# Kernel optimization log

Measured on AMD Instinct MI355X. Metric: run time of the kernel, lower is better.

## Reference

```python
import jax, jax.numpy as jnp
import numpy as np

B, C, H, W = 8, 256, 64, 64
CQK = C // 8


def setup_inputs() -> dict:
    key = jax.random.key(0)
    ks = jax.random.split(key, 9)
    s_in = 1.0 / np.sqrt(C)
    return {
        "feature1": jax.random.normal(ks[0], (B, C, H, W), jnp.float32),
        "feature2": jax.random.normal(ks[1], (B, C, H, W), jnp.float32),
        "feature3": jax.random.normal(ks[2], (B, C, H, W), jnp.float32),
        # 1x1 conv weights stored as [out_ch, in_ch]
        "wq": jax.random.uniform(ks[3], (CQK, C), jnp.float32, -s_in, s_in),
        "bq": jax.random.uniform(ks[4], (CQK,), jnp.float32, -s_in, s_in),
        "wk": jax.random.uniform(ks[5], (CQK, C), jnp.float32, -s_in, s_in),
        "bk": jax.random.uniform(ks[6], (CQK,), jnp.float32, -s_in, s_in),
        "wv": jax.random.uniform(ks[7], (C, C), jnp.float32, -s_in, s_in),
        "bv": jax.random.uniform(ks[8], (C,), jnp.float32, -s_in, s_in),
    }


def reference(feature1, feature2, feature3, wq, bq, wk, bk, wv, bv):
    b, c, h, w = feature1.shape
    hw = h * w
    # 1x1 convs == per-pixel channel GEMMs
    q = jnp.einsum('bchw,oc->bohw', feature1, wq) + bq[None, :, None, None]
    k = jnp.einsum('bchw,oc->bohw', feature2, wk) + bk[None, :, None, None]
    v = jnp.einsum('bchw,oc->bohw', feature3, wv) + bv[None, :, None, None]
    q = q.reshape(b, -1, hw).transpose(0, 2, 1)  # [b, hw, cqk]
    k = k.reshape(b, -1, hw)                      # [b, cqk, hw]
    v = v.reshape(b, -1, hw)                      # [b, c, hw]
    attn = jax.nn.softmax(jnp.einsum('bnc,bcm->bnm', q, k), axis=-1)  # [b, hw, hw]
    # fused = value @ attn^T  -> [b, c, hw]
    fused = jnp.einsum('bcm,bnm->bcn', v, attn)
    return fused.reshape(b, c, h, w)
```

## Files before the change

### kernel.cpp

```cpp
#include <hip/hip_runtime.h>
#include <math.h>

#define BATCH 8
#define CH    256
#define HWPIX 4096
#define CQK_  32

typedef __bf16 bf16x8 __attribute__((ext_vector_type(8)));
typedef __bf16 bf16x4 __attribute__((ext_vector_type(4)));
typedef __bf16 bf16x2 __attribute__((ext_vector_type(2)));
typedef float  f32x4  __attribute__((ext_vector_type(4)));

#define FS_STR 68

static __device__ inline bf16x8 ld_frag(const __bf16* p) {
  bf16x4 lo = *(const bf16x4*)p;
  bf16x4 hi = *(const bf16x4*)(p + 4);
  return __builtin_shufflevector(lo, hi, 0, 1, 2, 3, 4, 5, 6, 7);
}

static __device__ inline bf16x8 w_frag(const float* p) {
  const float4 a = *(const float4*)p;
  const float4 b = *(const float4*)(p + 4);
  bf16x8 r;
  r[0] = (__bf16)a.x; r[1] = (__bf16)a.y; r[2] = (__bf16)a.z; r[3] = (__bf16)a.w;
  r[4] = (__bf16)b.x; r[5] = (__bf16)b.y; r[6] = (__bf16)b.z; r[7] = (__bf16)b.w;
  return r;
}

__global__ __launch_bounds__(256, 4) void proj_all(
    const float* __restrict__ f1, const float* __restrict__ f2,
    const float* __restrict__ f3,
    const float* __restrict__ wq, const float* __restrict__ bq,
    const float* __restrict__ wk, const float* __restrict__ bk,
    const float* __restrict__ wv, const float* __restrict__ bv,
    __bf16* __restrict__ qT, __bf16* __restrict__ kT, __bf16* __restrict__ vv)
{
  __shared__ __align__(16) __bf16 f_s[2][64 * FS_STR];
  const int t    = threadIdx.x;
  const int w    = __builtin_amdgcn_readfirstlane(t >> 6);
  const int lane = t & 63;
  const int q16  = lane & 15;
  const int quad = lane >> 4;
  const int b    = blockIdx.z;
  const int n0   = blockIdx.x * 64;
  const int mode = blockIdx.y;

  const int sn  = (t & 15) * 4;
  const int scp = (t >> 4) * 2;
#define STAGE(fb, c0, dst)                                                      \
  {                                                                             \
    _Pragma("unroll") for (int rr = 0; rr < 2; ++rr) {                          \
      const int c = rr * 32 + scp;                                              \
      const float4 a0 = *(const float4*)&(fb)[(size_t)((c0) + c) * HWPIX + sn]; \
      const float4 a1 = *(const float4*)&(fb)[(size_t)((c0) + c + 1) * HWPIX + sn]; \
      _Pragma("unroll") for (int i = 0; i < 4; ++i) {                           \
        bf16x2 pk;                                                              \
        pk[0] = (__bf16)((const float*)&a0)[i];                                 \
        pk[1] = (__bf16)((const float*)&a1)[i];                                 \
        *(bf16x2*)&(dst)[(sn + i) * FS_STR + c] = pk;                           \
      }                                                                         \
    }                                                                           \
  }

  if (mode == 0) {
    const float* f1b = f1 + (size_t)b * CH * HWPIX + n0;
    const float* f2b = f2 + (size_t)b * CH * HWPIX + n0;
    f32x4 accQ[2], accK[2];
#pragma unroll
    for (int i = 0; i < 2; ++i) {
      accQ[i] = (f32x4){0.f, 0.f, 0.f, 0.f};
      accK[i] = (f32x4){0.f, 0.f, 0.f, 0.f};
    }
    for (int c0 = 0; c0 < CH; c0 += 64) {
      STAGE(f1b, c0, f_s[0]);
      STAGE(f2b, c0, f_s[1]);
      __syncthreads();
      bf16x8 afQ[2], afK[2];
#pragma unroll
      for (int kh = 0; kh < 2; ++kh) {
        afQ[kh] = ld_frag(&f_s[0][(16 * w + q16) * FS_STR + 32 * kh + quad * 8]);
        afK[kh] = ld_frag(&f_s[1][(16 * w + q16) * FS_STR + 32 * kh + quad * 8]);
      }
#pragma unroll
      for (int ot = 0; ot < 2; ++ot) {
#pragma unroll
        for (int kh = 0; kh < 2; ++kh) {
          const bf16x8 wfq =
              w_frag(wq + (size_t)(16 * ot + q16) * CH + c0 + 32 * kh + quad * 8);
          accQ[ot] = __builtin_amdgcn_mfma_f32_16x16x32_bf16(afQ[kh], wfq, accQ[ot], 0, 0, 0);
          const bf16x8 wfk =
              w_frag(wk + (size_t)(16 * ot + q16) * CH + c0 + 32 * kh + quad * 8);
          accK[ot] = __builtin_amdgcn_mfma_f32_16x16x32_bf16(afK[kh], wfk, accK[ot], 0, 0, 0);
        }
      }
      __syncthreads();
    }
    const float bq0 = bq[q16], bq1 = bq[16 + q16];
    const float bk0 = bk[q16], bk1 = bk[16 + q16];
#pragma unroll
    for (int r = 0; r < 4; ++r) {
      const size_t row = (size_t)b * HWPIX + n0 + 16 * w + quad * 4 + r;
      qT[row * CQK_ + q16]      = (__bf16)(accQ[0][r] + bq0);
      qT[row * CQK_ + 16 + q16] = (__bf16)(accQ[1][r] + bq1);
      kT[row * CQK_ + q16]      = (__bf16)(accK[0][r] + bk0);
      kT[row * CQK_ + 16 + q16] = (__bf16)(accK[1][r] + bk1);
    }
  } else {
    const int cbase = (mode - 1) * 128;
    const float* f3b = f3 + (size_t)b * CH * HWPIX + n0;
    f32x4 acc[2][4];
#pragma unroll
    for (int ct = 0; ct < 2; ++ct)
#pragma unroll
      for (int nt = 0; nt < 4; ++nt) acc[ct][nt] = (f32x4){0.f, 0.f, 0.f, 0.f};

    for (int c0 = 0; c0 < CH; c0 += 64) {
      STAGE(f3b, c0, f_s[0]);
      __syncthreads();
      bf16x8 af[2][2];
#pragma unroll
      for (int ct = 0; ct < 2; ++ct)
#pragma unroll
        for (int kh = 0; kh < 2; ++kh)
          af[ct][kh] = w_frag(wv + (size_t)(cbase + 64 * ct + 16 * w + q16) * CH
                              + c0 + 32 * kh + quad * 8);
#pragma unroll
      for (int nt = 0; nt < 4; ++nt) {
#pragma unroll
        for (int kh = 0; kh < 2; ++kh) {
          const bf16x8 bfr = ld_frag(&f_s[0][(16 * nt + q16) * FS_STR + 32 * kh + quad * 8]);
#pragma unroll
          for (int ct = 0; ct < 2; ++ct)
            acc[ct][nt] = __builtin_amdgcn_mfma_f32_16x16x32_bf16(
                af[ct][kh], bfr, acc[ct][nt], 0, 0, 0);
        }
      }
      __syncthreads();
    }
#pragma unroll
    for (int ct = 0; ct < 2; ++ct) {
      const float4 bi = *(const float4*)&bv[cbase + 64 * ct + 16 * w + quad * 4];
#pragma unroll
      for (int nt = 0; nt < 4; ++nt) {
#pragma unroll
        for (int r = 0; r < 4; ++r) {
          const int c = cbase + 64 * ct + 16 * w + quad * 4 + r;
          vv[((size_t)b * CH + c) * HWPIX + n0 + 16 * nt + q16] =
              (__bf16)(acc[ct][nt][r] + ((const float*)&bi)[r]);
        }
      }
    }
  }
#undef STAGE
}

__global__ __launch_bounds__(256, 2) void attn_kernel(
    const __bf16* __restrict__ qT, const __bf16* __restrict__ kT,
    const __bf16* __restrict__ vv, float* __restrict__ out)
{
  __shared__ __align__(16) __bf16 p_s[2][64 * 72];
  __shared__ float L_s[64];

  const int t    = threadIdx.x;
  const int w    = __builtin_amdgcn_readfirstlane(t >> 6);
  const int lane = t & 63;
  const int q16  = lane & 15;
  const int quad = lane >> 4;

  const int b  = blockIdx.x & 7;
  const int q0 = (blockIdx.x >> 3) * 64;

  const __bf16* kTb = kT + (size_t)b * HWPIX * CQK_;
  const int koff = q16 * CQK_ + quad * 8;

  const __bf16* vp[4];
#pragma unroll
  for (int ct = 0; ct < 4; ++ct)
    vp[ct] = vv + ((size_t)b * CH + 64 * w + 16 * ct + q16) * HWPIX + quad * 8;

  const bf16x8 qfrag =
      *(const bf16x8*)(qT + ((size_t)b * HWPIX + q0 + 16 * w + q16) * CQK_ + quad * 8);

  f32x4 oacc[4][4];
#pragma unroll
  for (int i = 0; i < 4; ++i)
#pragma unroll
    for (int j = 0; j < 4; ++j)
      oacc[i][j] = (f32x4){0.f, 0.f, 0.f, 0.f};
  float Lp[4] = {0.f, 0.f, 0.f, 0.f};

  bf16x8 kf[4];
#pragma unroll
  for (int mt = 0; mt < 4; ++mt)
    kf[mt] = *(const bf16x8*)(kTb + koff + mt * 512);
  {
    f32x4 Sv[4];
#pragma unroll
    for (int mt = 0; mt < 4; ++mt)
      Sv[mt] = __builtin_amdgcn_mfma_f32_16x16x32_bf16(
          qfrag, kf[mt], (f32x4){0.f, 0.f, 0.f, 0.f}, 0, 0, 0);
    const __bf16* kb1 = kTb + 64 * CQK_;
#pragma unroll
    for (int mt = 0; mt < 4; ++mt)
      kf[mt] = *(const bf16x8*)(kb1 + koff + mt * 512);
#pragma unroll
    for (int mt = 0; mt < 4; ++mt) {
#pragma unroll
      for (int r = 0; r < 4; ++r) {
        const float e = __expf(Sv[mt][r]);
        Lp[r] += e;
        p_s[0][(16 * w + quad * 4 + r) * 72 + 16 * mt + q16] = (__bf16)e;
      }
    }
  }
  __syncthreads();

  for (int i = 0; i < 64; ++i) {
    bf16x8 vf[4][2];
#pragma unroll
    for (int ct = 0; ct < 4; ++ct)
#pragma unroll
      for (int mh = 0; mh < 2; ++mh)
        vf[ct][mh] = *(const bf16x8*)(vp[ct] + mh * 32);

    const __bf16* pb = p_s[i & 1];
    bf16x8 pf[4][2];
#pragma unroll
    for (int nt = 0; nt < 4; ++nt)
#pragma unroll
      for (int mh = 0; mh < 2; ++mh)
        pf[nt][mh] = *(const bf16x8*)(&pb[(16 * nt + q16) * 72 + 32 * mh + quad * 8]);

    if (i < 63) {
      f32x4 Sv[4];
#pragma unroll
      for (int mt = 0; mt < 4; ++mt)
        Sv[mt] = __builtin_amdgcn_mfma_f32_16x16x32_bf16(
            qfrag, kf[mt], (f32x4){0.f, 0.f, 0.f, 0.f}, 0, 0, 0);
      const __bf16* kb2 = kTb + (size_t)((i + 2) & 63) * (64 * CQK_);
#pragma unroll
      for (int mt = 0; mt < 4; ++mt)
        kf[mt] = *(const bf16x8*)(kb2 + koff + mt * 512);
      __bf16* pw = p_s[(i + 1) & 1];
#pragma unroll
      for (int mt = 0; mt < 4; ++mt) {
#pragma unroll
        for (int r = 0; r < 4; ++r) {
          const float e = __expf(Sv[mt][r]);
          Lp[r] += e;
          pw[(16 * w + quad * 4 + r) * 72 + 16 * mt + q16] = (__bf16)e;
        }
      }
    }

#pragma unroll
    for (int ct = 0; ct < 4; ++ct)
#pragma unroll
      for (int nt = 0; nt < 4; ++nt)
#pragma unroll
        for (int mh = 0; mh < 2; ++mh)
          oacc[ct][nt] = __builtin_amdgcn_mfma_f32_16x16x32_bf16(
              vf[ct][mh], pf[nt][mh], oacc[ct][nt], 0, 0, 0);

#pragma unroll
    for (int ct = 0; ct < 4; ++ct) vp[ct] += 64;
    __syncthreads();
  }

#pragma unroll
  for (int r = 0; r < 4; ++r) {
    Lp[r] += __shfl_xor(Lp[r], 1);
    Lp[r] += __shfl_xor(Lp[r], 2);
    Lp[r] += __shfl_xor(Lp[r], 4);
    Lp[r] += __shfl_xor(Lp[r], 8);
  }
  if (q16 == 0) {
#pragma unroll
    for (int r = 0; r < 4; ++r) L_s[16 * w + quad * 4 + r] = Lp[r];
  }
  __syncthreads();

  float rinv[4];
#pragma unroll
  for (int nt = 0; nt < 4; ++nt) rinv[nt] = 1.0f / L_s[16 * nt + q16];

  float* ob = out + ((size_t)b * CH + 64 * w) * HWPIX + q0;
#pragma unroll
  for (int ct = 0; ct < 4; ++ct)
#pragma unroll
    for (int r = 0; r < 4; ++r)
#pragma unroll
      for (int nt = 0; nt < 4; ++nt)
        ob[(size_t)(16 * ct + quad * 4 + r) * HWPIX + 16 * nt + q16] =
            oacc[ct][nt][r] * rinv[nt];
}

extern "C" void kernel_launch(void* const* d_in, const int* in_sizes, int n_in,
                              void* d_out, int out_size, void* d_ws, size_t ws_size,
                              hipStream_t stream)
{
  const float* f1 = (const float*)d_in[0];
  const float* f2 = (const float*)d_in[1];
  const float* f3 = (const float*)d_in[2];
  const float* wq = (const float*)d_in[3];
  const float* bq = (const float*)d_in[4];
  const float* wk = (const float*)d_in[5];
  const float* bk = (const float*)d_in[6];
  const float* wv = (const float*)d_in[7];
  const float* bv = (const float*)d_in[8];
  float* outp = (float*)d_out;

  __bf16* qTw = (__bf16*)d_ws;
  __bf16* kTw = qTw + (size_t)BATCH * HWPIX * CQK_;
  __bf16* vw  = kTw + (size_t)BATCH * HWPIX * CQK_;

  proj_all<<<dim3(64, 3, 8), 256, 0, stream>>>(f1, f2, f3, wq, bq, wk, bk, wv, bv,
                                               qTw, kTw, vw);
  attn_kernel<<<dim3(512), 256, 0, stream>>>(qTw, kTw, vw, outp);
}
```

Baseline: 315.6 us.

## Split attention block across 8 waves with swizzled P tile and transposed S MFMA

The attention kernel now launches 512 threads per block. Each wave owns 32 output channels instead of 64, and the S computation is split across wave pairs, each covering half the key tile with operands swapped so results land in P's row-major layout. P is stored in shared memory with 8-byte vector writes and an XOR swizzle instead of padded scalar stores, and row sums are combined across the two half-waves at the end. This roughly halves the accumulator registers per wave and raises waves per CU, and it is meant to cut LDS bank conflicts. The cost is more block-level barrier participants and V being loaded by more waves.

```diff
diff --git a/kernel.cpp b/kernel.cpp
--- a/kernel.cpp
+++ b/kernel.cpp
@@ -155,107 +155,116 @@
 #undef STAGE
 }
 
-__global__ __launch_bounds__(256, 2) void attn_kernel(
+__global__ __launch_bounds__(512, 4) void attn_kernel(
     const __bf16* __restrict__ qT, const __bf16* __restrict__ kT,
     const __bf16* __restrict__ vv, float* __restrict__ out)
 {
-  __shared__ __align__(16) __bf16 p_s[2][64 * 72];
-  __shared__ float L_s[64];
+  __shared__ __align__(16) __bf16 p_s[2][64 * 64];
+  __shared__ float L_s[2][64];
 
   const int t    = threadIdx.x;
   const int w    = __builtin_amdgcn_readfirstlane(t >> 6);
   const int lane = t & 63;
   const int q16  = lane & 15;
   const int quad = lane >> 4;
+  const int qb   = w & 3;
+  const int hb   = w >> 2;
+  const int swz  = (q16 & 7) << 4;
 
   const int b  = blockIdx.x & 7;
   const int q0 = (blockIdx.x >> 3) * 64;
 
   const __bf16* kTb = kT + (size_t)b * HWPIX * CQK_;
-  const int koff = q16 * CQK_ + quad * 8;
-
-  const __bf16* vp[4];
-#pragma unroll
-  for (int ct = 0; ct < 4; ++ct)
-    vp[ct] = vv + ((size_t)b * CH + 64 * w + 16 * ct + q16) * HWPIX + quad * 8;
+  const size_t koff = (size_t)(32 * hb + q16) * CQK_ + quad * 8;
+
+  const __bf16* vp[2];
+#pragma unroll
+  for (int ct = 0; ct < 2; ++ct)
+    vp[ct] = vv + ((size_t)b * CH + 32 * w + 16 * ct + q16) * HWPIX + quad * 8;
 
   const bf16x8 qfrag =
-      *(const bf16x8*)(qT + ((size_t)b * HWPIX + q0 + 16 * w + q16) * CQK_ + quad * 8);
-
-  f32x4 oacc[4][4];
-#pragma unroll
-  for (int i = 0; i < 4; ++i)
+      *(const bf16x8*)(qT + ((size_t)b * HWPIX + q0 + 16 * qb + q16) * CQK_ + quad * 8);
+
+  f32x4 oacc[2][4];
+#pragma unroll
+  for (int i = 0; i < 2; ++i)
 #pragma unroll
     for (int j = 0; j < 4; ++j)
       oacc[i][j] = (f32x4){0.f, 0.f, 0.f, 0.f};
-  float Lp[4] = {0.f, 0.f, 0.f, 0.f};
-
-  bf16x8 kf[4];
-#pragma unroll
-  for (int mt = 0; mt < 4; ++mt)
+  float Lp = 0.f;
+
+  bf16x8 kf[2];
+#pragma unroll
+  for (int mt = 0; mt < 2; ++mt)
     kf[mt] = *(const bf16x8*)(kTb + koff + mt * 512);
   {
-    f32x4 Sv[4];
-#pragma unroll
-    for (int mt = 0; mt < 4; ++mt)
+    f32x4 Sv[2];
+#pragma unroll
+    for (int mt = 0; mt < 2; ++mt)
       Sv[mt] = __builtin_amdgcn_mfma_f32_16x16x32_bf16(
-          qfrag, kf[mt], (f32x4){0.f, 0.f, 0.f, 0.f}, 0, 0, 0);
+          kf[mt], qfrag, (f32x4){0.f, 0.f, 0.f, 0.f}, 0, 0, 0);
     const __bf16* kb1 = kTb + 64 * CQK_;
 #pragma unroll
-    for (int mt = 0; mt < 4; ++mt)
+    for (int mt = 0; mt < 2; ++mt)
       kf[mt] = *(const bf16x8*)(kb1 + koff + mt * 512);
-#pragma unroll
-    for (int mt = 0; mt < 4; ++mt) {
+    char* pw = (char*)p_s[0] + (16 * qb + q16) * 128;
+#pragma unroll
+    for (int mt = 0; mt < 2; ++mt) {
+      bf16x4 pk;
 #pragma unroll
       for (int r = 0; r < 4; ++r) {
         const float e = __expf(Sv[mt][r]);
-        Lp[r] += e;
-        p_s[0][(16 * w + quad * 4 + r) * 72 + 16 * mt + q16] = (__bf16)e;
-      }
+        Lp += e;
+        pk[r] = (__bf16)e;
+      }
+      *(bf16x4*)(pw + ((64 * hb + 32 * mt + 8 * quad) ^ swz)) = pk;
     }
   }
   __syncthreads();
 
   for (int i = 0; i < 64; ++i) {
-    bf16x8 vf[4][2];
-#pragma unroll
-    for (int ct = 0; ct < 4; ++ct)
+    bf16x8 vf[2][2];
+#pragma unroll
+    for (int ct = 0; ct < 2; ++ct)
 #pragma unroll
       for (int mh = 0; mh < 2; ++mh)
         vf[ct][mh] = *(const bf16x8*)(vp[ct] + mh * 32);
 
-    const __bf16* pb = p_s[i & 1];
+    const char* pb = (const char*)p_s[i & 1];
     bf16x8 pf[4][2];
 #pragma unroll
     for (int nt = 0; nt < 4; ++nt)
 #pragma unroll
       for (int mh = 0; mh < 2; ++mh)
-        pf[nt][mh] = *(const bf16x8*)(&pb[(16 * nt + q16) * 72 + 32 * mh + quad * 8]);
+        pf[nt][mh] = *(const bf16x8*)(pb + (16 * nt + q16) * 128
+                                      + ((64 * mh + 16 * quad) ^ swz));
 
     if (i < 63) {
-      f32x4 Sv[4];
-#pragma unroll
-      for (int mt = 0; mt < 4; ++mt)
+      f32x4 Sv[2];
+#pragma unroll
+      for (int mt = 0; mt < 2; ++mt)
         Sv[mt] = __builtin_amdgcn_mfma_f32_16x16x32_bf16(
-            qfrag, kf[mt], (f32x4){0.f, 0.f, 0.f, 0.f}, 0, 0, 0);
+            kf[mt], qfrag, (f32x4){0.f, 0.f, 0.f, 0.f}, 0, 0, 0);
       const __bf16* kb2 = kTb + (size_t)((i + 2) & 63) * (64 * CQK_);
 #pragma unroll
-      for (int mt = 0; mt < 4; ++mt)
+      for (int mt = 0; mt < 2; ++mt)
         kf[mt] = *(const bf16x8*)(kb2 + koff + mt * 512);
-      __bf16* pw = p_s[(i + 1) & 1];
-#pragma unroll
-      for (int mt = 0; mt < 4; ++mt) {
+      char* pw = (char*)p_s[(i + 1) & 1] + (16 * qb + q16) * 128;
+#pragma unroll
+      for (int mt = 0; mt < 2; ++mt) {
+        bf16x4 pk;
 #pragma unroll
         for (int r = 0; r < 4; ++r) {
           const float e = __expf(Sv[mt][r]);
-          Lp[r] += e;
-          pw[(16 * w + quad * 4 + r) * 72 + 16 * mt + q16] = (__bf16)e;
+          Lp += e;
+          pk[r] = (__bf16)e;
         }
-      }
-    }
-
-#pragma unroll
-    for (int ct = 0; ct < 4; ++ct)
+        *(bf16x4*)(pw + ((64 * hb + 32 * mt + 8 * quad) ^ swz)) = pk;
+      }
+    }
+
+#pragma unroll
+    for (int ct = 0; ct < 2; ++ct)
 #pragma unroll
       for (int nt = 0; nt < 4; ++nt)
 #pragma unroll
@@ -264,30 +273,23 @@
               vf[ct][mh], pf[nt][mh], oacc[ct][nt], 0, 0, 0);
 
 #pragma unroll
-    for (int ct = 0; ct < 4; ++ct) vp[ct] += 64;
+    for (int ct = 0; ct < 2; ++ct) vp[ct] += 64;
     __syncthreads();
   }
 
-#pragma unroll
-  for (int r = 0; r < 4; ++r) {
-    Lp[r] += __shfl_xor(Lp[r], 1);
-    Lp[r] += __shfl_xor(Lp[r], 2);
-    Lp[r] += __shfl_xor(Lp[r], 4);
-    Lp[r] += __shfl_xor(Lp[r], 8);
-  }
-  if (q16 == 0) {
-#pragma unroll
-    for (int r = 0; r < 4; ++r) L_s[16 * w + quad * 4 + r] = Lp[r];
-  }
+  Lp += __shfl_xor(Lp, 16);
+  Lp += __shfl_xor(Lp, 32);
+  if (quad == 0) L_s[hb][16 * qb + q16] = Lp;
   __syncthreads();
 
   float rinv[4];
 #pragma unroll
-  for (int nt = 0; nt < 4; ++nt) rinv[nt] = 1.0f / L_s[16 * nt + q16];
-
-  float* ob = out + ((size_t)b * CH + 64 * w) * HWPIX + q0;
-#pragma unroll
-  for (int ct = 0; ct < 4; ++ct)
+  for (int nt = 0; nt < 4; ++nt)
+    rinv[nt] = 1.0f / (L_s[0][16 * nt + q16] + L_s[1][16 * nt + q16]);
+
+  float* ob = out + ((size_t)b * CH + 32 * w) * HWPIX + q0;
+#pragma unroll
+  for (int ct = 0; ct < 2; ++ct)
 #pragma unroll
     for (int r = 0; r < 4; ++r)
 #pragma unroll
@@ -317,5 +319,5 @@
 
   proj_all<<<dim3(64, 3, 8), 256, 0, stream>>>(f1, f2, f3, wq, bq, wk, bk, wv, bv,
                                                qTw, kTw, vw);
-  attn_kernel<<<dim3(512), 256, 0, stream>>>(qTw, kTw, vw, outp);
-}
+  attn_kernel<<<dim3(512), 512, 0, stream>>>(qTw, kTw, vw, outp);
+}
```

New measurement: 315.2 us. No clear change (-0.1%).

## Rewrite attention kernel with 32x32 MFMA and register-only P, dropping LDS staging

Applied to the files above, without the earlier changes.

Switches the attention kernel from 16x16x32 MFMA with P staged through double-buffered LDS to 32x32x16 MFMA, where the S accumulator layout directly feeds the PV MFMA as a B operand. To make this work, the projection kernel writes K rows in a permuted order. Each wave then owns 32 queries and 128 channels and keeps P entirely in registers, which removes the LDS writes and reads, the per-iteration __syncthreads, and the cross-wave row-sum reduction. In exchange, each wave now recomputes S for its query tile redundantly (two waves share the same queries), and V and K are loaded directly from global memory with a register double buffer.

```diff
diff --git a/kernel.cpp b/kernel.cpp
--- a/kernel.cpp
+++ b/kernel.cpp
@@ -10,6 +10,7 @@
 typedef __bf16 bf16x4 __attribute__((ext_vector_type(4)));
 typedef __bf16 bf16x2 __attribute__((ext_vector_type(2)));
 typedef float  f32x4  __attribute__((ext_vector_type(4)));
+typedef float  f32x16 __attribute__((ext_vector_type(16)));
 
 #define FS_STR 68
 
@@ -100,11 +101,16 @@
     const float bk0 = bk[q16], bk1 = bk[16 + q16];
 #pragma unroll
     for (int r = 0; r < 4; ++r) {
-      const size_t row = (size_t)b * HWPIX + n0 + 16 * w + quad * 4 + r;
-      qT[row * CQK_ + q16]      = (__bf16)(accQ[0][r] + bq0);
-      qT[row * CQK_ + 16 + q16] = (__bf16)(accQ[1][r] + bq1);
-      kT[row * CQK_ + q16]      = (__bf16)(accK[0][r] + bk0);
-      kT[row * CQK_ + 16 + q16] = (__bf16)(accK[1][r] + bk1);
+      const size_t qrow = (size_t)b * HWPIX + n0 + 16 * w + quad * 4 + r;
+      qT[qrow * CQK_ + q16]      = (__bf16)(accQ[0][r] + bq0);
+      qT[qrow * CQK_ + 16 + q16] = (__bf16)(accQ[1][r] + bq1);
+      const int m   = 16 * (w & 1) + 4 * quad + r;
+      const int hik = (m >> 3) & 1;
+      const int rr  = (m & 7) + 8 * (m >> 4);
+      const int s   = (rr & 3) + 8 * (rr >> 2) + 4 * hik;
+      const size_t krow = (size_t)b * HWPIX + n0 + 32 * (w >> 1) + s;
+      kT[krow * CQK_ + q16]      = (__bf16)(accK[0][r] + bk0);
+      kT[krow * CQK_ + 16 + q16] = (__bf16)(accK[1][r] + bk1);
     }
   } else {
     const int cbase = (mode - 1) * 128;
@@ -159,141 +165,101 @@
     const __bf16* __restrict__ qT, const __bf16* __restrict__ kT,
     const __bf16* __restrict__ vv, float* __restrict__ out)
 {
-  __shared__ __align__(16) __bf16 p_s[2][64 * 72];
-  __shared__ float L_s[64];
-
   const int t    = threadIdx.x;
   const int w    = __builtin_amdgcn_readfirstlane(t >> 6);
   const int lane = t & 63;
-  const int q16  = lane & 15;
-  const int quad = lane >> 4;
+  const int lq   = lane & 31;
+  const int hi   = lane >> 5;
 
   const int b  = blockIdx.x & 7;
-  const int q0 = (blockIdx.x >> 3) * 64;
-
-  const __bf16* kTb = kT + (size_t)b * HWPIX * CQK_;
-  const int koff = q16 * CQK_ + quad * 8;
-
-  const __bf16* vp[4];
+  const int tl = blockIdx.x >> 3;
+  const int qbase  = tl * 64 + (w >> 1) * 32;
+  const int chbase = (w & 1) * 128;
+
+  const __bf16* kp = kT + (size_t)b * HWPIX * CQK_ + (size_t)lq * CQK_ + 8 * hi;
+  const __bf16* qp = qT + ((size_t)b * HWPIX + qbase + lq) * CQK_ + 8 * hi;
+  const __bf16* vp0 = vv + ((size_t)b * CH + chbase +  0 + lq) * HWPIX + 8 * hi;
+  const __bf16* vp1 = vp0 + (size_t)32 * HWPIX;
+  const __bf16* vp2 = vp0 + (size_t)64 * HWPIX;
+  const __bf16* vp3 = vp0 + (size_t)96 * HWPIX;
+
+  const bf16x8 qf0 = *(const bf16x8*)(qp);
+  const bf16x8 qf1 = *(const bf16x8*)(qp + 16);
+
+  f32x16 oacc[4];
 #pragma unroll
   for (int ct = 0; ct < 4; ++ct)
-    vp[ct] = vv + ((size_t)b * CH + 64 * w + 16 * ct + q16) * HWPIX + quad * 8;
-
-  const bf16x8 qfrag =
-      *(const bf16x8*)(qT + ((size_t)b * HWPIX + q0 + 16 * w + q16) * CQK_ + quad * 8);
-
-  f32x4 oacc[4][4];
-#pragma unroll
-  for (int i = 0; i < 4; ++i)
-#pragma unroll
-    for (int j = 0; j < 4; ++j)
-      oacc[i][j] = (f32x4){0.f, 0.f, 0.f, 0.f};
-  float Lp[4] = {0.f, 0.f, 0.f, 0.f};
-
-  bf16x8 kf[4];
-#pragma unroll
-  for (int mt = 0; mt < 4; ++mt)
-    kf[mt] = *(const bf16x8*)(kTb + koff + mt * 512);
-  {
-    f32x4 Sv[4];
-#pragma unroll
-    for (int mt = 0; mt < 4; ++mt)
-      Sv[mt] = __builtin_amdgcn_mfma_f32_16x16x32_bf16(
-          qfrag, kf[mt], (f32x4){0.f, 0.f, 0.f, 0.f}, 0, 0, 0);
-    const __bf16* kb1 = kTb + 64 * CQK_;
-#pragma unroll
-    for (int mt = 0; mt < 4; ++mt)
-      kf[mt] = *(const bf16x8*)(kb1 + koff + mt * 512);
-#pragma unroll
-    for (int mt = 0; mt < 4; ++mt) {
-#pragma unroll
-      for (int r = 0; r < 4; ++r) {
-        const float e = __expf(Sv[mt][r]);
-        Lp[r] += e;
-        p_s[0][(16 * w + quad * 4 + r) * 72 + 16 * mt + q16] = (__bf16)e;
-      }
-    }
-  }
-  __syncthreads();
-
-  for (int i = 0; i < 64; ++i) {
-    bf16x8 vf[4][2];
-#pragma unroll
-    for (int ct = 0; ct < 4; ++ct)
-#pragma unroll
-      for (int mh = 0; mh < 2; ++mh)
-        vf[ct][mh] = *(const bf16x8*)(vp[ct] + mh * 32);
-
-    const __bf16* pb = p_s[i & 1];
-    bf16x8 pf[4][2];
-#pragma unroll
-    for (int nt = 0; nt < 4; ++nt)
-#pragma unroll
-      for (int mh = 0; mh < 2; ++mh)
-        pf[nt][mh] = *(const bf16x8*)(&pb[(16 * nt + q16) * 72 + 32 * mh + quad * 8]);
-
-    if (i < 63) {
-      f32x4 Sv[4];
-#pragma unroll
-      for (int mt = 0; mt < 4; ++mt)
-        Sv[mt] = __builtin_amdgcn_mfma_f32_16x16x32_bf16(
-            qfrag, kf[mt], (f32x4){0.f, 0.f, 0.f, 0.f}, 0, 0, 0);
-      const __bf16* kb2 = kTb + (size_t)((i + 2) & 63) * (64 * CQK_);
-#pragma unroll
-      for (int mt = 0; mt < 4; ++mt)
-        kf[mt] = *(const bf16x8*)(kb2 + koff + mt * 512);
-      __bf16* pw = p_s[(i + 1) & 1];
-#pragma unroll
-      for (int mt = 0; mt < 4; ++mt) {
-#pragma unroll
-        for (int r = 0; r < 4; ++r) {
-          const float e = __expf(Sv[mt][r]);
-          Lp[r] += e;
-          pw[(16 * w + quad * 4 + r) * 72 + 16 * mt + q16] = (__bf16)e;
-        }
-      }
-    }
-
-#pragma unroll
-    for (int ct = 0; ct < 4; ++ct)
-#pragma unroll
-      for (int nt = 0; nt < 4; ++nt)
-#pragma unroll
-        for (int mh = 0; mh < 2; ++mh)
-          oacc[ct][nt] = __builtin_amdgcn_mfma_f32_16x16x32_bf16(
-              vf[ct][mh], pf[nt][mh], oacc[ct][nt], 0, 0, 0);
-
-#pragma unroll
-    for (int ct = 0; ct < 4; ++ct) vp[ct] += 64;
-    __syncthreads();
-  }
-
-#pragma unroll
-  for (int r = 0; r < 4; ++r) {
-    Lp[r] += __shfl_xor(Lp[r], 1);
-    Lp[r] += __shfl_xor(Lp[r], 2);
-    Lp[r] += __shfl_xor(Lp[r], 4);
-    Lp[r] += __shfl_xor(Lp[r], 8);
-  }
-  if (q16 == 0) {
-#pragma unroll
-    for (int r = 0; r < 4; ++r) L_s[16 * w + quad * 4 + r] = Lp[r];
-  }
-  __syncthreads();
-
-  float rinv[4];
-#pragma unroll
-  for (int nt = 0; nt < 4; ++nt) rinv[nt] = 1.0f / L_s[16 * nt + q16];
-
-  float* ob = out + ((size_t)b * CH + 64 * w) * HWPIX + q0;
+#pragma unroll
+    for (int r = 0; r < 16; ++r) oacc[ct][r] = 0.f;
+  float Lp = 0.f;
+
+  bf16x8 kA0, kA1, kB0, kB1;
+  bf16x8 vA[4][2], vB[4][2];
+  kA0 = *(const bf16x8*)(kp);
+  kA1 = *(const bf16x8*)(kp + 16);
+  vA[0][0] = *(const bf16x8*)(vp0);      vA[0][1] = *(const bf16x8*)(vp0 + 16);
+  vA[1][0] = *(const bf16x8*)(vp1);      vA[1][1] = *(const bf16x8*)(vp1 + 16);
+  vA[2][0] = *(const bf16x8*)(vp2);      vA[2][1] = *(const bf16x8*)(vp2 + 16);
+  vA[3][0] = *(const bf16x8*)(vp3);      vA[3][1] = *(const bf16x8*)(vp3 + 16);
+
+  const f32x16 z16 = {0.f,0.f,0.f,0.f,0.f,0.f,0.f,0.f,
+                      0.f,0.f,0.f,0.f,0.f,0.f,0.f,0.f};
+
+#define STEP(KB, CK0, CK1, CV, NK0, NK1, NV)                                    \
+  {                                                                             \
+    const int kn = ((KB) + 1) & 127;                                            \
+                           \
+    NK0 = *(const bf16x8*)(kp + (size_t)kn * 1024);                             \
+    NK1 = *(const bf16x8*)(kp + (size_t)kn * 1024 + 16);                        \
+    NV[0][0] = *(const bf16x8*)(vp0 + kn * 32);                                 \
+    NV[0][1] = *(const bf16x8*)(vp0 + kn * 32 + 16);                            \
+    NV[1][0] = *(const bf16x8*)(vp1 + kn * 32);                                 \
+    NV[1][1] = *(const bf16x8*)(vp1 + kn * 32 + 16);                            \
+    NV[2][0] = *(const bf16x8*)(vp2 + kn * 32);                                 \
+    NV[2][1] = *(const bf16x8*)(vp2 + kn * 32 + 16);                            \
+    NV[3][0] = *(const bf16x8*)(vp3 + kn * 32);                                 \
+    NV[3][1] = *(const bf16x8*)(vp3 + kn * 32 + 16);                            \
+                       \
+    f32x16 Sv = __builtin_amdgcn_mfma_f32_32x32x16_bf16(CK0, qf0, z16, 0, 0, 0);\
+    Sv = __builtin_amdgcn_mfma_f32_32x32x16_bf16(CK1, qf1, Sv, 0, 0, 0);        \
+              \
+    bf16x8 pf0, pf1;                                                            \
+    _Pragma("unroll") for (int j = 0; j < 8; ++j) {                             \
+      const float e = __expf(Sv[j]);                                            \
+      Lp += e;                                                                  \
+      pf0[j] = (__bf16)e;                                                       \
+    }                                                                           \
+    _Pragma("unroll") for (int j = 0; j < 8; ++j) {                             \
+      const float e = __expf(Sv[8 + j]);                                        \
+      Lp += e;                                                                  \
+      pf1[j] = (__bf16)e;                                                       \
+    }                                                                           \
+                                                      \
+    _Pragma("unroll") for (int ct = 0; ct < 4; ++ct) {                          \
+      oacc[ct] = __builtin_amdgcn_mfma_f32_32x32x16_bf16(CV[ct][0], pf0,        \
+                                                         oacc[ct], 0, 0, 0);    \
+      oacc[ct] = __builtin_amdgcn_mfma_f32_32x32x16_bf16(CV[ct][1], pf1,        \
+                                                         oacc[ct], 0, 0, 0);    \
+    }                                                                           \
+  }
+
+  for (int kb = 0; kb < 128; kb += 2) {
+    STEP(kb,     kA0, kA1, vA, kB0, kB1, vB);
+    STEP(kb + 1, kB0, kB1, vB, kA0, kA1, vA);
+  }
+#undef STEP
+
+  Lp += __shfl_xor(Lp, 32);
+  const float rinv = 1.0f / Lp;
+
+  float* ob = out + ((size_t)b * CH + chbase) * HWPIX + qbase + lq;
 #pragma unroll
   for (int ct = 0; ct < 4; ++ct)
 #pragma unroll
-    for (int r = 0; r < 4; ++r)
-#pragma unroll
-      for (int nt = 0; nt < 4; ++nt)
-        ob[(size_t)(16 * ct + quad * 4 + r) * HWPIX + 16 * nt + q16] =
-            oacc[ct][nt][r] * rinv[nt];
+    for (int r = 0; r < 16; ++r) {
+      const int ch = 32 * ct + (r & 3) + 8 * (r >> 2) + 4 * hi;
+      ob[(size_t)ch * HWPIX] = oacc[ct][r] * rinv;
+    }
 }
 
 extern "C" void kernel_launch(void* const* d_in, const int* in_sizes, int n_in,
```

Result: slower. 427.2 us (+35.4%).
